# Kernel tuning notes

Hardware: AMD Instinct MI355X
Metric: run time of the kernel (lower is better)

## Reference

```python
import jax, jax.numpy as jnp
import numpy as np

NUM_CLASSES = 20
FC = 512  # feature_channels
H = W = 28


def _conv(x, w, b):
    y = jax.lax.conv_general_dilated(x, w, (1, 1), 'SAME',
                                     dimension_numbers=('NCHW', 'OIHW', 'NCHW'))
    return y + b[None, :, None, None]


def _center_map(centers, height, width):
    # centers: [B, N, 4] = (x, y, class, conf); vectorized scatter replacing the python loop
    B, N, _ = centers.shape
    xp = (centers[..., 0] * width).astype(jnp.int32)   # int() truncation; x>=0 so == floor
    yp = (centers[..., 1] * height).astype(jnp.int32)
    conf = centers[..., 3]
    valid = (xp >= 0) & (xp < width) & (yp >= 0) & (yp < height)
    flat = jnp.where(valid, yp * width + xp, height * width)  # invalid -> dummy slot
    m = jnp.zeros((B, height * width + 1), centers.dtype)
    m = m.at[jnp.arange(B)[:, None], flat].set(conf)
    return m[:, :height * width].reshape(B, 1, height, width)


def setup_inputs() -> dict:
    key = jax.random.key(0)
    ks = jax.random.split(key, 16)
    B = 256
    image = jax.random.normal(ks[0], (B, 3, H, W), jnp.float32)
    features = jax.random.normal(ks[1], (B, FC, 7, 7), jnp.float32)
    centers = jax.random.uniform(ks[2], (B, 100, 4), jnp.float32)

    def conv_w(k, co, ci):
        s = 1.0 / np.sqrt(ci * 9)
        return jax.random.uniform(k, (co, ci, 3, 3), jnp.float32, -s, s)

    def lin_w(k, co, ci):
        s = 1.0 / np.sqrt(ci)
        return jax.random.uniform(k, (co, ci), jnp.float32, -s, s)

    cin = FC + 3 + 1  # 516
    return {
        'image': image, 'features': features, 'centers': centers,
        'w1': conv_w(ks[3], 128, cin), 'b1': jnp.zeros((128,), jnp.float32),
        'w2': conv_w(ks[4], 64, 128), 'b2': jnp.zeros((64,), jnp.float32),
        'w3': conv_w(ks[5], 32, 64), 'b3': jnp.zeros((32,), jnp.float32),
        'w4': conv_w(ks[6], 16, 32), 'b4': jnp.zeros((16,), jnp.float32),
        'fw1': lin_w(ks[7], 256, 16 * H * W), 'fb1': jnp.zeros((256,), jnp.float32),
        'fw2': lin_w(ks[8], 4 + NUM_CLASSES, 256), 'fb2': jnp.zeros((4 + NUM_CLASSES,), jnp.float32),
    }


def reference(image, features, centers, w1, b1, w2, b2, w3, b3, w4, b4, fw1, fb1, fw2, fb2):
    B = image.shape[0]
    feats = jax.image.resize(features, (B, FC, H, W), method='bilinear')  # align_corners=False
    cmap = _center_map(centers, H, W)
    x = jnp.concatenate([image, feats, cmap], axis=1)  # [B, 516, 28, 28]
    x = jax.nn.relu(_conv(x, w1, b1))
    x = jax.nn.relu(_conv(x, w2, b2))
    x = jax.nn.relu(_conv(x, w3, b3))
    x = jax.nn.relu(_conv(x, w4, b4))
    x = x.reshape(B, -1)
    x = jax.nn.relu(x @ fw1.T + fb1)
    action = x @ fw2.T + fb2  # [B, 4 + num_classes]
    action = action.at[:, 2].set(jax.nn.sigmoid(action[:, 2]))
    action = action.at[:, 3].set(jax.nn.sigmoid(action[:, 3]))
    return action
```

## Files before the change

### kernel.cpp

```cpp
#include <hip/hip_runtime.h>

typedef _Float16 f16;
typedef _Float16 f16x8 __attribute__((ext_vector_type(8)));
typedef float    f32x4 __attribute__((ext_vector_type(4)));

static __device__ __forceinline__ f16x8 ld8(const f16* p) {
    return *reinterpret_cast<const f16x8*>(p);
}

static constexpr size_t W1T_B  = 1253376;
static constexpr size_t W2T_B  = 147456;
static constexpr size_t W3T_B  = 36864;
static constexpr size_t W4T_B  = 9216;
static constexpr size_t FW1T_B = 6422528;
static constexpr size_t WEIGHTS_B = W1T_B + W2T_B + W3T_B + W4T_B + FW1T_B;

static constexpr size_t PB_X0 = 979200;
static constexpr size_t PB_X1 = 230400;
static constexpr size_t PB_X2 = 115200;
static constexpr size_t PB_X3 = 57600;
static constexpr size_t PB_X4 = 25088;
static constexpr size_t PB_X5 = 512;
static constexpr size_t PER_BATCH = PB_X0 + PB_X1 + PB_X2 + PB_X3 + PB_X4 + PB_X5;

static __device__ __forceinline__ void wxf(const float* __restrict__ w, f16* __restrict__ wt,
                                           int i, int CINr, int NCB, int COUT) {
    int co = i % COUT;
    int r  = i / COUT;
    int hi = r & 3; r >>= 2;
    int cb = r % NCB;
    int tap = r / NCB;
    f16x8 v;
    #pragma unroll
    for (int j = 0; j < 8; ++j) {
        int ci = cb * 32 + hi * 8 + j;
        float x = (ci < CINr) ? w[((size_t)co * CINr + ci) * 9 + tap] : 0.f;
        v[j] = (f16)x;
    }
    *reinterpret_cast<f16x8*>(wt + (size_t)i * 8) = v;
}

static constexpr int S1 = 9 * 17 * 4 * 128;
static constexpr int S2 = 9 * 4  * 4 * 64;
static constexpr int S3 = 9 * 2  * 4 * 32;
static constexpr int S4 = 9 * 1  * 4 * 16;
static constexpr int SW = S1 + S2 + S3 + S4;
static constexpr int SFW = 256 * 12544;
static constexpr int PREP_TOT = SW + SFW;

__global__ void prep_all(const float* __restrict__ w1, const float* __restrict__ w2,
                         const float* __restrict__ w3, const float* __restrict__ w4,
                         const float* __restrict__ fw1,
                         f16* __restrict__ W1t, f16* __restrict__ W2t,
                         f16* __restrict__ W3t, f16* __restrict__ W4t,
                         f16* __restrict__ FW1t) {
    int t = blockIdx.x * 256 + threadIdx.x;
    if (t >= PREP_TOT) return;
    if (t < S1) { wxf(w1, W1t, t, 516, 17, 128); return; }
    t -= S1;
    if (t < S2) { wxf(w2, W2t, t, 128, 4, 64); return; }
    t -= S2;
    if (t < S3) { wxf(w3, W3t, t, 64, 2, 32); return; }
    t -= S3;
    if (t < S4) { wxf(w4, W4t, t, 32, 1, 16); return; }
    t -= S4;
    int o = t / 12544, idx = t % 12544;
    int y = idx / 448, rem = idx % 448;
    int x = rem / 16, c = rem & 15;
    FW1t[t] = (f16)fw1[(size_t)o * 12544 + c * 784 + y * 28 + x];
}

static __device__ __forceinline__ void ring_yx(int bi, int& y, int& x) {
    if (bi < 30)      { y = 0;        x = bi; }
    else if (bi < 60) { y = 29;       x = bi - 30; }
    else if (bi < 88) { y = bi - 59;  x = 0; }
    else              { y = bi - 87;  x = 29; }
}

__global__ __launch_bounds__(512) void build_x0(
        const float* __restrict__ img, const float* __restrict__ feat,
        const float* __restrict__ centers,
        f16* __restrict__ X0, f16* __restrict__ X1,
        f16* __restrict__ X2, f16* __restrict__ X3, int b0) {
    const int bl = blockIdx.x;
    const int b  = b0 + bl;
    const int tid = threadIdx.x;
    f16* x0b = X0 + (size_t)bl * (17 * 900 * 32);

    for (int i = tid; i < 116 * 544; i += 512) {
        int c = i % 544, bi = i / 544;
        int y, x; ring_yx(bi, y, x);
        x0b[((size_t)(c >> 5) * 900 + y * 30 + x) * 32 + (c & 31)] = (f16)0.f;
    }
    for (int i = tid; i < 784; i += 512) {
        int y = i / 28, x = i % 28;
        x0b[((size_t)16 * 900 + (y + 1) * 30 + x + 1) * 32 + 3] = (f16)0.f;
    }
    for (int i = tid; i < 3 * 784; i += 512) {
        int c = i / 784, p = i % 784;
        int y = p / 28, x = p % 28;
        x0b[((size_t)(y + 1) * 30 + x + 1) * 32 + c] =
            (f16)img[((size_t)b * 3 + c) * 784 + p];
    }
    {
        const int c  = tid + 3;
        const int cb = c >> 5, c32 = c & 31;
        const float* fb = feat + ((size_t)b * 512 + tid) * 49;
        float r0[7], r1[7];
        int cur = -100;
        for (int y = 0; y < 28; ++y) {
            float sy = (y + 0.5f) * 0.25f - 0.5f;
            float fy = floorf(sy);
            int iy0 = (int)fy;
            float wy1 = sy - fy, wy0 = 1.f - wy1;
            if (iy0 != cur) {
                cur = iy0;
                int i0 = iy0 < 0 ? 0 : iy0;
                int i1 = (iy0 + 1 > 6) ? 6 : iy0 + 1;
                #pragma unroll
                for (int j = 0; j < 7; ++j) { r0[j] = fb[i0 * 7 + j]; r1[j] = fb[i1 * 7 + j]; }
            }
            f16* orow = x0b + ((size_t)cb * 900 + (y + 1) * 30 + 1) * 32 + c32;
            #pragma unroll 28
            for (int x = 0; x < 28; ++x) {
                float sx = (x + 0.5f) * 0.25f - 0.5f;
                float fx = floorf(sx);
                int ix0 = (int)fx;
                float wx1 = sx - fx, wx0 = 1.f - wx1;
                int j0 = ix0 < 0 ? 0 : ix0;
                int j1 = (ix0 + 1 > 6) ? 6 : ix0 + 1;
                float v = wy0 * (wx0 * r0[j0] + wx1 * r0[j1]) +
                          wy1 * (wx0 * r1[j0] + wx1 * r1[j1]);
                orow[(size_t)x * 32] = (f16)v;
            }
        }
    }
    {
        f16* x1b = X1 + (size_t)bl * (4 * 900 * 32);
        for (int i = tid; i < 116 * 128; i += 512) {
            int c = i % 128, bi = i / 128;
            int y, x; ring_yx(bi, y, x);
            x1b[((size_t)(c >> 5) * 900 + y * 30 + x) * 32 + (c & 31)] = (f16)0.f;
        }
        f16* x2b = X2 + (size_t)bl * (2 * 900 * 32);
        for (int i = tid; i < 116 * 64; i += 512) {
            int c = i % 64, bi = i / 64;
            int y, x; ring_yx(bi, y, x);
            x2b[((size_t)(c >> 5) * 900 + y * 30 + x) * 32 + (c & 31)] = (f16)0.f;
        }
        f16* x3b = X3 + (size_t)bl * (900 * 32);
        for (int i = tid; i < 116 * 32; i += 512) {
            int c = i % 32, bi = i / 32;
            int y, x; ring_yx(bi, y, x);
            x3b[((size_t)y * 30 + x) * 32 + c] = (f16)0.f;
        }
    }
    __syncthreads();
    if (tid == 0) {
        const float* cb = centers + (size_t)b * 400;
        for (int n = 0; n < 100; ++n) {
            float cx = cb[n * 4 + 0], cy = cb[n * 4 + 1], conf = cb[n * 4 + 3];
            int xp = (int)(cx * 28.f);
            int yp = (int)(cy * 28.f);
            if (xp >= 0 && xp < 28 && yp >= 0 && yp < 28)
                x0b[((size_t)16 * 900 + (yp + 1) * 30 + xp + 1) * 32 + 3] = (f16)conf;
        }
    }
}

template<int CIN, int COUT, int GM, int GN, int WNT, int MW, bool PADOUT>
__global__ __launch_bounds__(512) void conv3x3(const f16* __restrict__ Xin,
                                               const f16* __restrict__ Wt,
                                               const float* __restrict__ bias,
                                               f16* __restrict__ Xout) {
    constexpr int NCB  = CIN / 32;
    constexpr int NCBO = COUT / 32;
    constexpr int NV_B = 9 * 4 * COUT;
    __shared__ f16 Bs[NV_B * 8];

    const int rg = blockIdx.x;
    const int b  = blockIdx.y;
    const int tid = threadIdx.x;
    const int wave = tid >> 6;
    const int lane = tid & 63;
    const int lm = lane & 15, hi = lane >> 4;
    const int wm = wave % GM, wn = wave / GM;
    const int MT = (rg < 3) ? 14 : 7;

    f32x4 acc[MW][WNT];
    #pragma unroll
    for (int k = 0; k < MW; ++k)
        #pragma unroll
        for (int n = 0; n < WNT; ++n)
            acc[k][n] = (f32x4){0.f, 0.f, 0.f, 0.f};

    const size_t bbase = (size_t)b * NCB * 900;
    int inoff[MW];
    #pragma unroll
    for (int k = 0; k < MW; ++k) {
        const int m = wm + k * GM;
        const int p = m * 16 + lm;
        const int yl = p / 28, x = p - yl * 28;
        inoff[k] = (m < MT) ? ((rg * 8 + yl) * 30 + x) : 0;
    }

    for (int cb = 0; cb < NCB; ++cb) {
        for (int v = tid; v < NV_B; v += 512) {
            const int tap = v / (4 * COUT);
            const int w   = v - tap * (4 * COUT);
            *reinterpret_cast<f16x8*>(Bs + (size_t)v * 8) =
                ld8(Wt + ((size_t)(tap * NCB + cb) * (4 * COUT) + w) * 8);
        }
        __syncthreads();

        #pragma unroll
        for (int tap = 0; tap < 9; ++tap) {
            f16x8 bf[WNT];
            #pragma unroll
            for (int n = 0; n < WNT; ++n)
                bf[n] = *reinterpret_cast<const f16x8*>(
                    Bs + ((size_t)(tap * 4 + hi) * COUT + (wn * WNT + n) * 16 + lm) * 8);
            const int dy = tap / 3, dx = tap - dy * 3;
            const size_t dOff = (bbase + (size_t)cb * 900 + dy * 30 + dx) * 32 + hi * 8;
            #pragma unroll
            for (int k = 0; k < MW; ++k) {
                if (wm + k * GM < MT) {
                    const f16x8 af = ld8(Xin + dOff + (size_t)inoff[k] * 32);
                    #pragma unroll
                    for (int n = 0; n < WNT; ++n)
                        acc[k][n] = __builtin_amdgcn_mfma_f32_16x16x32_f16(af, bf[n], acc[k][n], 0, 0, 0);
                }
            }
        }
        __syncthreads();
    }

    #pragma unroll
    for (int k = 0; k < MW; ++k) {
        const int m = wm + k * GM;
        if (m < MT) {
            #pragma unroll
            for (int n = 0; n < WNT; ++n) {
                const int co = (wn * WNT + n) * 16 + lm;
                const float bv = bias[co];
                #pragma unroll
                for (int r = 0; r < 4; ++r) {
                    const int p = m * 16 + hi * 4 + r;
                    const int yl = p / 28, x = p - yl * 28;
                    const float v = fmaxf(acc[k][n][r] + bv, 0.f);
                    size_t off;
                    if (PADOUT)
                        off = (((size_t)b * NCBO + (co >> 5)) * 900 +
                               (rg * 8 + yl + 1) * 30 + (x + 1)) * 32 + (co & 31);
                    else
                        off = ((size_t)b * 784 + (rg * 8 + yl) * 28 + x) * COUT + co;
                    Xout[off] = (f16)v;
                }
            }
        }
    }
}

__global__ __launch_bounds__(256) void fc1k(const f16* __restrict__ X4,
                                            const f16* __restrict__ FW1t,
                                            const float* __restrict__ fb1,
                                            f16* __restrict__ X5, int CH) {
    const int bm = blockIdx.x;
    const int nt = blockIdx.y * 4 + (threadIdx.x >> 6);
    const int lane = threadIdx.x & 63;
    const int lm = lane & 15, hi = lane >> 4;
    f32x4 acc = (f32x4){0.f, 0.f, 0.f, 0.f};
    const int row0 = bm * 16 + lm;
    const int rowA = (row0 < CH) ? row0 : 0;
    const f16* arow = X4 + (size_t)rowA * 12544;
    const int o = nt * 16 + lm;
    const f16* brow = FW1t + (size_t)o * 12544;
    for (int kk = 0; kk < 12544; kk += 32) {
        const f16x8 af = ld8(arow + kk + hi * 8);
        const f16x8 bf = ld8(brow + kk + hi * 8);
        acc = __builtin_amdgcn_mfma_f32_16x16x32_f16(af, bf, acc, 0, 0, 0);
    }
    const float bv = fb1[o];
    #pragma unroll
    for (int r = 0; r < 4; ++r) {
        const int row = bm * 16 + hi * 4 + r;
        if (row < CH)
            X5[(size_t)row * 256 + o] = (f16)fmaxf(acc[r] + bv, 0.f);
    }
}

__global__ void fc2k(const f16* __restrict__ X5, const float* __restrict__ fw2,
                     const float* __restrict__ fb2, float* __restrict__ out, int CH) {
    int t = blockIdx.x * 256 + threadIdx.x;
    if (t < CH * 24) {
        int b = t / 24, o = t % 24;
        float s = fb2[o];
        const f16* xr = X5 + (size_t)b * 256;
        const float* wr = fw2 + (size_t)o * 256;
        for (int k = 0; k < 256; ++k) s += (float)xr[k] * wr[k];
        if (o == 2 || o == 3) s = 1.f / (1.f + expf(-s));
        out[t] = s;
    }
}

extern "C" void kernel_launch(void* const* d_in, const int* in_sizes, int n_in,
                              void* d_out, int out_size, void* d_ws, size_t ws_size,
                              hipStream_t stream) {
    const float* image    = (const float*)d_in[0];
    const float* features = (const float*)d_in[1];
    const float* centers  = (const float*)d_in[2];
    const float* w1  = (const float*)d_in[3];
    const float* b1  = (const float*)d_in[4];
    const float* w2  = (const float*)d_in[5];
    const float* b2  = (const float*)d_in[6];
    const float* w3  = (const float*)d_in[7];
    const float* b3  = (const float*)d_in[8];
    const float* w4  = (const float*)d_in[9];
    const float* b4  = (const float*)d_in[10];
    const float* fw1 = (const float*)d_in[11];
    const float* fb1 = (const float*)d_in[12];
    const float* fw2 = (const float*)d_in[13];
    const float* fb2 = (const float*)d_in[14];

    int CH = 8;
    for (int c = 256; c >= 8; c >>= 1) {
        if (WEIGHTS_B + (size_t)c * PER_BATCH <= ws_size) { CH = c; break; }
    }

    char* ws = (char*)d_ws;
    f16* W1t  = (f16*)(ws);
    f16* W2t  = (f16*)(ws + W1T_B);
    f16* W3t  = (f16*)(ws + W1T_B + W2T_B);
    f16* W4t  = (f16*)(ws + W1T_B + W2T_B + W3T_B);
    f16* FW1t = (f16*)(ws + W1T_B + W2T_B + W3T_B + W4T_B);
    char* act = ws + WEIGHTS_B;
    f16* X0 = (f16*)(act);
    f16* X1 = (f16*)(act + (size_t)CH * PB_X0);
    f16* X2 = (f16*)(act + (size_t)CH * (PB_X0 + PB_X1));
    f16* X3 = (f16*)(act + (size_t)CH * (PB_X0 + PB_X1 + PB_X2));
    f16* X4 = (f16*)(act + (size_t)CH * (PB_X0 + PB_X1 + PB_X2 + PB_X3));
    f16* X5 = (f16*)(act + (size_t)CH * (PB_X0 + PB_X1 + PB_X2 + PB_X3 + PB_X4));

    prep_all<<<(PREP_TOT + 255) / 256, 256, 0, stream>>>(w1, w2, w3, w4, fw1,
                                                         W1t, W2t, W3t, W4t, FW1t);

    for (int b0 = 0; b0 < 256; b0 += CH) {
        build_x0<<<CH, 512, 0, stream>>>(image, features, centers,
                                         X0, X1, X2, X3, b0);

        dim3 cgrid(4, CH);
        conv3x3<544, 128, 4, 2, 4, 4, true ><<<cgrid, 512, 0, stream>>>(X0, W1t, b1, X1);
        conv3x3<128, 64,  4, 2, 2, 4, true ><<<cgrid, 512, 0, stream>>>(X1, W2t, b2, X2);
        conv3x3<64,  32,  4, 2, 1, 4, true ><<<cgrid, 512, 0, stream>>>(X2, W3t, b3, X3);
        conv3x3<32,  16,  8, 1, 1, 2, false><<<cgrid, 512, 0, stream>>>(X3, W4t, b4, X4);

        dim3 fgrid((CH + 15) / 16, 4);
        fc1k<<<fgrid, 256, 0, stream>>>(X4, FW1t, fb1, X5, CH);
        fc2k<<<(CH * 24 + 255) / 256, 256, 0, stream>>>(X5, fw2, fb2,
                                                        (float*)d_out + (size_t)b0 * 24, CH);
    }
}
```

Measured before the change: 874.7 us.

## Double-buffer conv weight panels in LDS with register prefetch

The weight panel for the next input-channel block is loaded from global memory into registers before the MFMA loop over taps runs, then written into a second LDS buffer afterwards. This leaves one barrier per iteration instead of two and hides global load latency behind compute. In exchange it doubles the LDS footprint and adds staging registers per thread, which could lower occupancy for the larger COUT variants.

```diff
diff --git a/kernel.cpp b/kernel.cpp
--- a/kernel.cpp
+++ b/kernel.cpp
@@ -176,7 +176,8 @@
     constexpr int NCB  = CIN / 32;
     constexpr int NCBO = COUT / 32;
     constexpr int NV_B = 9 * 4 * COUT;
-    __shared__ f16 Bs[NV_B * 8];
+    constexpr int PT   = (NV_B + 511) / 512;
+    __shared__ f16 Bs[2][NV_B * 8];
 
     const int rg = blockIdx.x;
     const int b  = blockIdx.y;
@@ -204,22 +205,45 @@
         inoff[k] = (m < MT) ? ((rg * 8 + yl) * 30 + x) : 0;
     }
 
-    for (int cb = 0; cb < NCB; ++cb) {
-        for (int v = tid; v < NV_B; v += 512) {
+    f16x8 st[PT];
+    #pragma unroll
+    for (int pi = 0; pi < PT; ++pi) {
+        const int v = tid + pi * 512;
+        if (v < NV_B) {
             const int tap = v / (4 * COUT);
             const int w   = v - tap * (4 * COUT);
-            *reinterpret_cast<f16x8*>(Bs + (size_t)v * 8) =
-                ld8(Wt + ((size_t)(tap * NCB + cb) * (4 * COUT) + w) * 8);
-        }
-        __syncthreads();
-
+            st[pi] = ld8(Wt + ((size_t)(tap * NCB) * (4 * COUT) + w) * 8);
+        }
+    }
+    #pragma unroll
+    for (int pi = 0; pi < PT; ++pi) {
+        const int v = tid + pi * 512;
+        if (v < NV_B)
+            *reinterpret_cast<f16x8*>(&Bs[0][0] + (size_t)v * 8) = st[pi];
+    }
+    __syncthreads();
+
+    int cur = 0;
+    for (int cb = 0; cb < NCB; ++cb) {
+        if (cb + 1 < NCB) {
+            #pragma unroll
+            for (int pi = 0; pi < PT; ++pi) {
+                const int v = tid + pi * 512;
+                if (v < NV_B) {
+                    const int tap = v / (4 * COUT);
+                    const int w   = v - tap * (4 * COUT);
+                    st[pi] = ld8(Wt + ((size_t)(tap * NCB + cb + 1) * (4 * COUT) + w) * 8);
+                }
+            }
+        }
+        const f16* bpan = &Bs[cur][0];
         #pragma unroll
         for (int tap = 0; tap < 9; ++tap) {
             f16x8 bf[WNT];
             #pragma unroll
             for (int n = 0; n < WNT; ++n)
                 bf[n] = *reinterpret_cast<const f16x8*>(
-                    Bs + ((size_t)(tap * 4 + hi) * COUT + (wn * WNT + n) * 16 + lm) * 8);
+                    bpan + ((size_t)(tap * 4 + hi) * COUT + (wn * WNT + n) * 16 + lm) * 8);
             const int dy = tap / 3, dx = tap - dy * 3;
             const size_t dOff = (bbase + (size_t)cb * 900 + dy * 30 + dx) * 32 + hi * 8;
             #pragma unroll
@@ -232,7 +256,17 @@
                 }
             }
         }
+        if (cb + 1 < NCB) {
+            f16* bnxt = &Bs[cur ^ 1][0];
+            #pragma unroll
+            for (int pi = 0; pi < PT; ++pi) {
+                const int v = tid + pi * 512;
+                if (v < NV_B)
+                    *reinterpret_cast<f16x8*>(bnxt + (size_t)v * 8) = st[pi];
+            }
+        }
         __syncthreads();
+        cur ^= 1;
     }
 
     #pragma unroll
```

Result: slower. 948.5 us (+8.4%).
